# Optimization experiments

Measured on AMD Instinct MI355X. Metric: run time of the kernel, lower is better.

The kernel has to match this reference:

```python
import jax, jax.numpy as jnp
import numpy as np

B, IN, OUT, RANK = 256, 1024, 1024, 16


def setup_inputs() -> dict:
    key = jax.random.key(0)
    k1, k2, k3, k4 = jax.random.split(key, 4)
    std = (0.02 * RANK ** (-0.5)) ** 0.5
    return {
        "input": jax.random.normal(k1, (B, IN), dtype=jnp.float32),
        "coef": jax.random.normal(k2, (B, RANK), dtype=jnp.float32),
        "weight": jax.random.normal(k3, (OUT, IN, RANK), dtype=jnp.float32) * std,
        "bias": jax.random.normal(k4, (OUT, RANK), dtype=jnp.float32) * 0.02,
    }


def reference(input, coef, weight, bias):
    # Per-sample path of MixtureLinear (coef has shape (B, rank), B > 1):
    # out[b,o] = sum_i input[b,i] * sum_r weight[o,i,r] * coef[b,r]
    #          + sum_r bias[o,r] * coef[b,r]
    # Fused form: contract input with weight first -> (B, out, rank), a tiny
    # intermediate, instead of materializing the (B, out, in) combined weight.
    proj = jnp.einsum('bi,oir->bor', input, weight)   # (B, OUT, RANK)
    out = jnp.einsum('bor,br->bo', proj, coef)         # (B, OUT)
    out = out + jnp.einsum('or,br->bo', bias, coef)
    return out
```

## Files before the change

kernel.cpp:

```cpp
#include <hip/hip_runtime.h>
#include <hip/hip_bf16.h>

#define M 256
#define NOUT 1024
#define KTOT 16384
#define IN 1024
#define RANK 16
#define NKC 32
#define KCHUNK 512
#define NPH 16

typedef __attribute__((ext_vector_type(8)))  short bf16x8_t;
typedef __attribute__((ext_vector_type(4)))  float f32x4_t;
typedef __attribute__((ext_vector_type(16))) float f32x16_t;
typedef __attribute__((ext_vector_type(8)))  unsigned short u16x8_t;
typedef __attribute__((ext_vector_type(4)))  unsigned short u16x4_t;

static __device__ __forceinline__ unsigned short f2bf(float f) {
  unsigned u = __builtin_bit_cast(unsigned, f);
  u += 0x7FFFu + ((u >> 16) & 1u);
  return (unsigned short)(u >> 16);
}
static __device__ __forceinline__ float bf2f(unsigned short h) {
  unsigned u = ((unsigned)h) << 16;
  return __builtin_bit_cast(float, u);
}
static __device__ __forceinline__ void dsw4(unsigned short* dst, float4 v) {
  u16x4_t h;
  h[0] = f2bf(v.x); h[1] = f2bf(v.y); h[2] = f2bf(v.z); h[3] = f2bf(v.w);
  *(u16x4_t*)dst = h;
}

__global__ __launch_bounds__(512, 2) void gemm_kernel(
    const float* __restrict__ input, const float* __restrict__ coef,
    const float* __restrict__ W, unsigned short* __restrict__ part)
{
  __shared__ float          in_lds[256 * 33];
  __shared__ __align__(16) unsigned short Ws[2][2048];

  const int tid = threadIdx.x;
  const int wid = tid >> 6, lane = tid & 63;
  const int l31 = lane & 31, l5 = lane >> 5;
  const int bq = wid >> 1, oc = wid & 1;
  const int bbase = bq * 64;

  const int lin = blockIdx.y * 16 + blockIdx.x;
  const int swb = (lin & 7) * 64 + (lin >> 3);
  const int ot = swb & 15, kc = swb >> 4;

  const int o0 = ot * 64;
  const int kb0 = kc * KCHUNK;
  const int i0 = kc * 32;

  f32x16_t acc0 = (f32x16_t)(0.0f), acc1 = (f32x16_t)(0.0f);

  {
    int b = tid >> 1, half = tid & 1;
    const float* src = input + (size_t)b * IN + i0 + half * 16;
    float* dst = in_lds + b * 33 + half * 16;
    #pragma unroll
    for (int j = 0; j < 16; ++j) dst[j] = src[j];
  }

  float c0[8], c1[8];
  {
    const float* cp0 = coef + (size_t)(bbase + l31) * RANK + l5 * 8;
    const float* cp1 = coef + (size_t)(bbase + 32 + l31) * RANK + l5 * 8;
    #pragma unroll
    for (int e = 0; e < 8; ++e) { c0[e] = cp0[e]; c1[e] = cp1[e]; }
  }

  const int wo = tid >> 3, wk4 = (tid & 7) * 4;
  const float* wgp = W + (size_t)(o0 + wo) * KTOT + kb0 + wk4;
  const int wdst = ((((tid & 7) >> 1) * 64 + wo) * 8 + (tid & 1) * 4);

  float4 wA, wB;

  #define LOADW(S, P) { w##S = *(const float4*)(wgp + (P) * 32); }
  #define DSW(S, BUF) dsw4(&Ws[BUF][wdst], w##S);

  #define KSTEP(TL, BUF)                                                     \
    {                                                                        \
      int i = (TL);                                                          \
      float in0 = in_lds[(bbase + l31) * 33 + i];                            \
      float in1 = in_lds[(bbase + 32 + l31) * 33 + i];                       \
      bf16x8_t af0, af1;                                                     \
      _Pragma("unroll")                                                      \
      for (int e = 0; e < 8; ++e) {                                          \
        af0[e] = (short)f2bf(in0 * c0[e]);                                   \
        af1[e] = (short)f2bf(in1 * c1[e]);                                   \
      }                                                                      \
      bf16x8_t bf = *(const bf16x8_t*)                                       \
          &Ws[BUF][((((TL) & 1) * 2 + l5) * 64 + oc * 32 + l31) * 8];        \
      __builtin_amdgcn_s_setprio(1);                                         \
      acc0 = __builtin_amdgcn_mfma_f32_32x32x16_bf16(af0, bf, acc0, 0, 0, 0);\
      acc1 = __builtin_amdgcn_mfma_f32_32x32x16_bf16(af1, bf, acc1, 0, 0, 0);\
      __builtin_amdgcn_s_setprio(0);                                         \
    }

  #define PHASE(P, SC, SN, DOL)                                              \
    if (DOL) { LOADW(SC, (P) + 2) }                                          \
    KSTEP((P) * 2,     (P) & 1)                                              \
    KSTEP((P) * 2 + 1, (P) & 1)                                              \
    if ((P) + 1 < NPH) { DSW(SN, ((P) + 1) & 1) }                            \
    __syncthreads();

  LOADW(A, 0)
  LOADW(B, 1)
  DSW(A, 0)
  __syncthreads();

  PHASE(0,  A, B, 1)  PHASE(1,  B, A, 1)  PHASE(2,  A, B, 1)  PHASE(3,  B, A, 1)
  PHASE(4,  A, B, 1)  PHASE(5,  B, A, 1)  PHASE(6,  A, B, 1)  PHASE(7,  B, A, 1)
  PHASE(8,  A, B, 1)  PHASE(9,  B, A, 1)  PHASE(10, A, B, 1)  PHASE(11, B, A, 1)
  PHASE(12, A, B, 1)  PHASE(13, B, A, 1)  PHASE(14, A, B, 0)  PHASE(15, B, A, 0)

  unsigned short* pp = part + (size_t)kc * (M * NOUT);
  #pragma unroll
  for (int q = 0; q < 16; ++q) {
    int brow = bbase + (q & 3) + 8 * (q >> 2) + 4 * l5;
    int ocol = o0 + oc * 32 + l31;
    pp[(size_t)brow * NOUT + ocol]        = f2bf(acc0[q]);
    pp[(size_t)(brow + 32) * NOUT + ocol] = f2bf(acc1[q]);
  }
  #undef LOADW
  #undef DSW
  #undef KSTEP
  #undef PHASE
}

__global__ __launch_bounds__(256) void reduce_bias_kernel(
    const unsigned short* __restrict__ part, const float* __restrict__ bias,
    const float* __restrict__ coef, float* __restrict__ out)
{
  int t = blockIdx.x * 256 + threadIdx.x;
  int idx8 = t * 8;
  int b = idx8 >> 10, o = idx8 & 1023;

  float s[8];
  #pragma unroll
  for (int j = 0; j < 8; ++j) s[j] = 0.f;

  #pragma unroll
  for (int c = 0; c < NKC; ++c) {
    u16x8_t v = *(const u16x8_t*)(part + (size_t)c * (M * NOUT) + idx8);
    #pragma unroll
    for (int j = 0; j < 8; ++j) s[j] += bf2f(v[j]);
  }

  const f32x4_t* cr = (const f32x4_t*)(coef + (size_t)b * RANK);
  f32x4_t c0 = cr[0], c1 = cr[1], c2 = cr[2], c3 = cr[3];
  #pragma unroll
  for (int j = 0; j < 8; ++j) {
    const f32x4_t* br = (const f32x4_t*)(bias + (size_t)(o + j) * RANK);
    f32x4_t b0 = br[0], b1 = br[1], b2 = br[2], b3 = br[3];
    float bb = 0.f;
    #pragma unroll
    for (int e = 0; e < 4; ++e)
      bb += b0[e] * c0[e] + b1[e] * c1[e] + b2[e] * c2[e] + b3[e] * c3[e];
    s[j] += bb;
  }
  float4* dst = (float4*)(out + idx8);
  dst[0] = make_float4(s[0], s[1], s[2], s[3]);
  dst[1] = make_float4(s[4], s[5], s[6], s[7]);
}

extern "C" void kernel_launch(void* const* d_in, const int* in_sizes, int n_in,
                              void* d_out, int out_size, void* d_ws, size_t ws_size,
                              hipStream_t stream) {
  const float* input = (const float*)d_in[0];
  const float* coef  = (const float*)d_in[1];
  const float* W     = (const float*)d_in[2];
  const float* bias  = (const float*)d_in[3];
  float* out = (float*)d_out;

  unsigned short* part = (unsigned short*)d_ws;

  gemm_kernel<<<dim3(16, 32), 512, 0, stream>>>(input, coef, W, part);
  reduce_bias_kernel<<<(M * NOUT) / (256 * 8), 256, 0, stream>>>(part, bias, coef, out);
}
```

Baseline: 34.00 us.

## Halve pipeline phases, use packed bf16 converts, and use lighter barriers

Each phase now stages 64 K-columns of W per buffer instead of 32, so the block runs 8 phases and 8 barriers instead of 16. Each thread loads two float4s per phase. The software bf16 rounding is replaced with the hardware v_cvt_pk_bf16_f32 instruction for both the A-fragment construction and the W staging. __syncthreads is replaced with an explicit lgkmcnt wait, s_barrier and sched_barriers, and the launch-bounds occupancy hint is raised to 4. In exchange the double-buffered W tile in LDS doubles in size, register pressure per thread rises, and the sched_barriers constrain how the compiler can schedule instructions.

Result: faster. 31.21 us (-8.2%).

```diff
diff --git a/kernel.cpp b/kernel.cpp
--- a/kernel.cpp
+++ b/kernel.cpp
@@ -8,13 +8,12 @@
 #define RANK 16
 #define NKC 32
 #define KCHUNK 512
-#define NPH 16
+#define NPH 8
 
 typedef __attribute__((ext_vector_type(8)))  short bf16x8_t;
 typedef __attribute__((ext_vector_type(4)))  float f32x4_t;
 typedef __attribute__((ext_vector_type(16))) float f32x16_t;
 typedef __attribute__((ext_vector_type(8)))  unsigned short u16x8_t;
-typedef __attribute__((ext_vector_type(4)))  unsigned short u16x4_t;
 
 static __device__ __forceinline__ unsigned short f2bf(float f) {
   unsigned u = __builtin_bit_cast(unsigned, f);
@@ -25,18 +24,30 @@
   unsigned u = ((unsigned)h) << 16;
   return __builtin_bit_cast(float, u);
 }
-static __device__ __forceinline__ void dsw4(unsigned short* dst, float4 v) {
-  u16x4_t h;
-  h[0] = f2bf(v.x); h[1] = f2bf(v.y); h[2] = f2bf(v.z); h[3] = f2bf(v.w);
-  *(u16x4_t*)dst = h;
+static __device__ __forceinline__ unsigned cvtpk1(float lo, float hi) {
+  unsigned r;
+  asm("v_cvt_pk_bf16_f32 %0, %1, %2" : "=v"(r) : "v"(lo), "v"(hi));
+  return r;
+}
+static __device__ __forceinline__ bf16x8_t mulcvt8(float s, const float* c) {
+  union { bf16x8_t v; unsigned u[4]; } r;
+  #pragma unroll
+  for (int e = 0; e < 4; ++e)
+    r.u[e] = cvtpk1(s * c[2 * e], s * c[2 * e + 1]);
+  return r.v;
+}
+static __device__ __forceinline__ void dsw4pk(unsigned short* dst, float4 v) {
+  unsigned a = cvtpk1(v.x, v.y), b = cvtpk1(v.z, v.w);
+  unsigned long long q = ((unsigned long long)b << 32) | (unsigned long long)a;
+  *(unsigned long long*)dst = q;
 }
 
-__global__ __launch_bounds__(512, 2) void gemm_kernel(
+__global__ __launch_bounds__(512, 4) void gemm_kernel(
     const float* __restrict__ input, const float* __restrict__ coef,
     const float* __restrict__ W, unsigned short* __restrict__ part)
 {
-  __shared__ float          in_lds[256 * 33];
-  __shared__ __align__(16) unsigned short Ws[2][2048];
+  __shared__ float in_lds[256 * 33];
+  __shared__ __align__(16) unsigned short Ws[2][4096];
 
   const int tid = threadIdx.x;
   const int wid = tid >> 6, lane = tid & 63;
@@ -69,29 +80,35 @@
     #pragma unroll
     for (int e = 0; e < 8; ++e) { c0[e] = cp0[e]; c1[e] = cp1[e]; }
   }
+  const int ib0 = (bbase + l31) * 33, ib1 = (bbase + 32 + l31) * 33;
 
-  const int wo = tid >> 3, wk4 = (tid & 7) * 4;
-  const float* wgp = W + (size_t)(o0 + wo) * KTOT + kb0 + wk4;
-  const int wdst = ((((tid & 7) >> 1) * 64 + wo) * 8 + (tid & 1) * 4);
+  const float* wgp0 = W + (size_t)(o0 + (tid >> 4)) * KTOT + kb0 + (tid & 15) * 4;
+  const float* wgp1 = wgp0 + (size_t)32 * KTOT;
+  const int wd0 = ((((tid & 15) >> 1) * 64 + (tid >> 4)) * 8 + (tid & 1) * 4);
+  const int wd1 = wd0 + 32 * 8;
 
-  float4 wA, wB;
+  float4 wA0, wA1, wB0, wB1;
 
-  #define LOADW(S, P) { w##S = *(const float4*)(wgp + (P) * 32); }
-  #define DSW(S, BUF) dsw4(&Ws[BUF][wdst], w##S);
+  #define SB __builtin_amdgcn_sched_barrier(0);
+  #define BARX                                                               \
+    SB asm volatile("s_waitcnt lgkmcnt(0)" ::: "memory");                    \
+    __builtin_amdgcn_s_barrier(); SB
+
+  #define LOADW(S, P)                                                        \
+    { w##S##0 = *(const float4*)(wgp0 + (P) * 64);                           \
+      w##S##1 = *(const float4*)(wgp1 + (P) * 64); }
+
+  #define DSW2(S, BUF)                                                       \
+    { dsw4pk(&Ws[BUF][wd0], w##S##0); dsw4pk(&Ws[BUF][wd1], w##S##1); }
 
   #define KSTEP(TL, BUF)                                                     \
     {                                                                        \
-      int i = (TL);                                                          \
-      float in0 = in_lds[(bbase + l31) * 33 + i];                            \
-      float in1 = in_lds[(bbase + 32 + l31) * 33 + i];                       \
-      bf16x8_t af0, af1;                                                     \
-      _Pragma("unroll")                                                      \
-      for (int e = 0; e < 8; ++e) {                                          \
-        af0[e] = (short)f2bf(in0 * c0[e]);                                   \
-        af1[e] = (short)f2bf(in1 * c1[e]);                                   \
-      }                                                                      \
+      float in0 = in_lds[ib0 + (TL)];                                        \
+      float in1 = in_lds[ib1 + (TL)];                                        \
+      bf16x8_t af0 = mulcvt8(in0, c0);                                       \
+      bf16x8_t af1 = mulcvt8(in1, c1);                                       \
       bf16x8_t bf = *(const bf16x8_t*)                                       \
-          &Ws[BUF][((((TL) & 1) * 2 + l5) * 64 + oc * 32 + l31) * 8];        \
+          &Ws[BUF][((((TL) & 3) * 2 + l5) * 64 + oc * 32 + l31) * 8];        \
       __builtin_amdgcn_s_setprio(1);                                         \
       acc0 = __builtin_amdgcn_mfma_f32_32x32x16_bf16(af0, bf, acc0, 0, 0, 0);\
       acc1 = __builtin_amdgcn_mfma_f32_32x32x16_bf16(af1, bf, acc1, 0, 0, 0);\
@@ -100,20 +117,18 @@
 
   #define PHASE(P, SC, SN, DOL)                                              \
     if (DOL) { LOADW(SC, (P) + 2) }                                          \
-    KSTEP((P) * 2,     (P) & 1)                                              \
-    KSTEP((P) * 2 + 1, (P) & 1)                                              \
-    if ((P) + 1 < NPH) { DSW(SN, ((P) + 1) & 1) }                            \
-    __syncthreads();
+    KSTEP((P) * 4,     (P) & 1)  KSTEP((P) * 4 + 1, (P) & 1)                 \
+    KSTEP((P) * 4 + 2, (P) & 1)  KSTEP((P) * 4 + 3, (P) & 1)                 \
+    if ((P) + 1 < NPH) { DSW2(SN, ((P) + 1) & 1) }                           \
+    BARX
 
   LOADW(A, 0)
   LOADW(B, 1)
-  DSW(A, 0)
-  __syncthreads();
+  DSW2(A, 0)
+  BARX
 
-  PHASE(0,  A, B, 1)  PHASE(1,  B, A, 1)  PHASE(2,  A, B, 1)  PHASE(3,  B, A, 1)
-  PHASE(4,  A, B, 1)  PHASE(5,  B, A, 1)  PHASE(6,  A, B, 1)  PHASE(7,  B, A, 1)
-  PHASE(8,  A, B, 1)  PHASE(9,  B, A, 1)  PHASE(10, A, B, 1)  PHASE(11, B, A, 1)
-  PHASE(12, A, B, 1)  PHASE(13, B, A, 1)  PHASE(14, A, B, 0)  PHASE(15, B, A, 0)
+  PHASE(0, A, B, 1)  PHASE(1, B, A, 1)  PHASE(2, A, B, 1)  PHASE(3, B, A, 1)
+  PHASE(4, A, B, 1)  PHASE(5, B, A, 1)  PHASE(6, A, B, 0)  PHASE(7, B, A, 0)
 
   unsigned short* pp = part + (size_t)kc * (M * NOUT);
   #pragma unroll
@@ -124,9 +139,11 @@
     pp[(size_t)(brow + 32) * NOUT + ocol] = f2bf(acc1[q]);
   }
   #undef LOADW
-  #undef DSW
+  #undef DSW2
   #undef KSTEP
   #undef PHASE
+  #undef BARX
+  #undef SB
 }
 
 __global__ __launch_bounds__(256) void reduce_bias_kernel(
```
